# Kernel tuning notes

Hardware: AMD Instinct MI355X
Metric: run time of the kernel (lower is better)

The kernel has to match this reference:

```python
import jax, jax.numpy as jnp
import numpy as np
from jax import lax

M, N, Q = 256, 65536, 64
LAMBDA_STAR = 0.1
LAMBDA_O = 0.1
T_ITERS = 16
PM_ITERS = 100


def setup_inputs() -> dict:
    key = jax.random.key(0)
    kx, kd = jax.random.split(key)
    X = jax.random.normal(kx, (M, N), dtype=jnp.float32)
    D = jax.random.normal(kd, (M, Q), dtype=jnp.float32)
    return {"X": X, "D": D}


def _power_method(D):
    # Largest eigenvalue of D^T D via 100-step power iteration (fixed random init).
    x0 = jax.random.normal(jax.random.key(1), (1, Q), dtype=D.dtype)

    def step(x, _):
        x = (x @ D.T) @ D          # [1,q] -> [1,m] -> [1,q]
        nm = jnp.linalg.norm(x)
        return x / nm, nm

    _, nms = lax.scan(step, x0, None, length=PM_ITERS)
    return nms[-1]


def reference(X, D):
    m, n = X.shape
    q = D.shape[1]
    alpha = _power_method(D)
    eta = 1.0 / alpha

    Iq = jnp.eye(q, dtype=D.dtype)
    Im = jnp.eye(m, dtype=D.dtype)
    top = jnp.concatenate([D.T @ D + LAMBDA_STAR * Iq, D.T], axis=1)   # [q, q+m]
    bot = jnp.concatenate([D, (1.0 + LAMBDA_STAR) * Im], axis=1)       # [m, q+m]
    H = jnp.eye(m + q, dtype=D.dtype) - eta * jnp.concatenate([top, bot], axis=0)
    W = eta * jnp.concatenate([D.T, Im], axis=0)                        # [(m+q), m]
    t = LAMBDA_O * eta * jnp.concatenate([jnp.zeros(q, D.dtype), jnp.ones(m, D.dtype)])

    b0 = W @ X                                                           # [(m+q), n]
    Z0 = jnp.zeros((m + q, n), dtype=X.dtype)

    def ista_step(carry, _):
        Z, b = carry
        Znew = jnp.maximum(0.0, b - t[:, None])    # thresholding (ger(t, ones) == t broadcast)
        b = b + H @ (Znew - Z)
        return (Znew, b), None

    (Z, _), _ = lax.scan(ista_step, (Z0, b0), None, length=T_ITERS)
    return Z
```

## Files before the change

### kernel.cpp

```cpp
#include <hip/hip_runtime.h>


typedef __bf16 bf16x8 __attribute__((ext_vector_type(8)));
typedef __bf16 bf16x2 __attribute__((ext_vector_type(2)));
typedef float f32x4 __attribute__((ext_vector_type(4)));
typedef float f32x2 __attribute__((ext_vector_type(2)));

#define MFMA16(a, b, c) __builtin_amdgcn_mfma_f32_16x16x32_bf16((a), (b), (c), 0, 0, 0)

#define NTOT 65536
#define NCOL 32

__device__ __forceinline__ unsigned pk2(float a, float b) {
#if __has_builtin(__builtin_amdgcn_cvt_pk_bf16_f32)
  return __builtin_bit_cast(unsigned, __builtin_amdgcn_cvt_pk_bf16_f32(a, b));
#else
  unsigned short ua = __builtin_bit_cast(unsigned short, (__bf16)a);
  unsigned short ub = __builtin_bit_cast(unsigned short, (__bf16)b);
  return (unsigned)ua | ((unsigned)ub << 16);
#endif
}
__device__ __forceinline__ unsigned pk2v(f32x2 v) { return pk2(v[0], v[1]); }
__device__ __forceinline__ f32x2 f2(float s) { f32x2 v = {s, s}; return v; }
__device__ __forceinline__ f32x2 pfma(f32x2 a, f32x2 b, f32x2 c) {
  return __builtin_elementwise_fma(a, b, c);
}
__device__ __forceinline__ f32x2 pmax0(f32x2 a) {
  return __builtin_elementwise_max(a, f2(0.f));
}

#define GOF(row) ((row) * 68 + (((row) >> 3) << 2))
__global__ void rnmf_prep(const float* __restrict__ D, void* __restrict__ ws) {
  float* wsf = (float*)ws;
  __bf16* Dbf = (__bf16*)((char*)ws + 256);
  __bf16* DTbf = (__bf16*)((char*)ws + 256 + 32768);

  const int tid = threadIdx.x;

  if (blockIdx.x != 0) {
    const int bs = blockIdx.x - 1;
#pragma unroll
    for (int e = 0; e < 8; ++e) {
      int i4 = bs * 2048 + e * 256 + tid;
      float4 dv = *(const float4*)(D + i4 * 4);
      uint2 u; u.x = pk2(dv.x, dv.y); u.y = pk2(dv.z, dv.w);
      *(uint2*)(Dbf + i4 * 4) = u;
    }
    const int a = tid & 63;
#pragma unroll
    for (int e = 0; e < 4; ++e) {
      int kc = bs * 16 + e * 4 + (tid >> 6);
      int k0 = kc * 8;
      float g0 = D[(k0 + 0) * 64 + a], g1 = D[(k0 + 1) * 64 + a];
      float g2 = D[(k0 + 2) * 64 + a], g3 = D[(k0 + 3) * 64 + a];
      float g4 = D[(k0 + 4) * 64 + a], g5 = D[(k0 + 5) * 64 + a];
      float g6 = D[(k0 + 6) * 64 + a], g7 = D[(k0 + 7) * 64 + a];
      uint4 o;
      o.x = pk2(g0, g1); o.y = pk2(g2, g3); o.z = pk2(g4, g5); o.w = pk2(g6, g7);
      *(uint4*)(DTbf + a * 256 + k0) = o;
    }
    return;
  }

  __shared__ __bf16 DTl[64 * 264];
  __shared__ __bf16 gA[64 * 72];
  __shared__ __bf16 gB[64 * 72];
  __shared__ float gf[64 * 68 + 32];
  __shared__ __align__(16) float xv[64];

  const int w = tid >> 6, lane = tid & 63, c = lane & 15, q4 = lane >> 4;

#pragma unroll
  for (int e = 0; e < 64; ++e) {
    int flat = e * 256 + tid;
    int k = flat >> 6, a = flat & 63;
    DTl[a * 264 + k] = (__bf16)D[k * 64 + a];
  }
  __syncthreads();
#pragma unroll
  for (int ct = 0; ct < 4; ++ct) {
    f32x4 acc = {0.f, 0.f, 0.f, 0.f};
#pragma unroll
    for (int kb = 0; kb < 8; ++kb) {
      bf16x8 a = *(const bf16x8*)&DTl[(16 * w + c) * 264 + 32 * kb + 8 * q4];
      bf16x8 b = *(const bf16x8*)&DTl[(16 * ct + c) * 264 + 32 * kb + 8 * q4];
      acc = MFMA16(a, b, acc);
    }
#pragma unroll
    for (int r = 0; r < 4; ++r)
      gA[(16 * w + 4 * q4 + r) * 72 + 16 * ct + c] = (__bf16)acc[r];
  }
  __syncthreads();
#pragma unroll
  for (int ct = 0; ct < 4; ++ct) {
    f32x4 acc = {0.f, 0.f, 0.f, 0.f};
#pragma unroll
    for (int kb = 0; kb < 2; ++kb) {
      bf16x8 a = *(const bf16x8*)&gA[(16 * w + c) * 72 + 32 * kb + 8 * q4];
      bf16x8 b = *(const bf16x8*)&gA[(16 * ct + c) * 72 + 32 * kb + 8 * q4];
      acc = MFMA16(a, b, acc);
    }
#pragma unroll
    for (int r = 0; r < 4; ++r)
      gB[(16 * w + 4 * q4 + r) * 72 + 16 * ct + c] = (__bf16)acc[r];
  }
  __syncthreads();
#pragma unroll
  for (int ct = 0; ct < 4; ++ct) {
    f32x4 acc = {0.f, 0.f, 0.f, 0.f};
#pragma unroll
    for (int kb = 0; kb < 2; ++kb) {
      bf16x8 a = *(const bf16x8*)&gB[(16 * w + c) * 72 + 32 * kb + 8 * q4];
      bf16x8 b = *(const bf16x8*)&gB[(16 * ct + c) * 72 + 32 * kb + 8 * q4];
      acc = MFMA16(a, b, acc);
    }
#pragma unroll
    for (int r = 0; r < 4; ++r)
      gA[(16 * w + 4 * q4 + r) * 72 + 16 * ct + c] = (__bf16)acc[r];
  }
  __syncthreads();
#pragma unroll
  for (int ct = 0; ct < 4; ++ct) {
    f32x4 acc = {0.f, 0.f, 0.f, 0.f};
#pragma unroll
    for (int kb = 0; kb < 2; ++kb) {
      bf16x8 a = *(const bf16x8*)&gA[(16 * w + c) * 72 + 32 * kb + 8 * q4];
      bf16x8 b = *(const bf16x8*)&gA[(16 * ct + c) * 72 + 32 * kb + 8 * q4];
      acc = MFMA16(a, b, acc);
    }
#pragma unroll
    for (int r = 0; r < 4; ++r)
      gf[GOF(16 * w + 4 * q4 + r) + 16 * ct + c] = acc[r];
  }
  __syncthreads();

  if (w == 0) {
    float td = gf[GOF(lane) + lane];
#pragma unroll
    for (int off = 32; off; off >>= 1) td += __shfl_xor(td, off, 64);
    const float tr = td;
    const float itr = 1.f / tr;
    xv[lane] = 1.f;
    float nm = 1.f;
    const int rowoff = GOF(lane);
    for (int itp = 0; itp < 28; ++itp) {
      float a0 = 0.f, a1 = 0.f, a2 = 0.f, a3 = 0.f;
#pragma unroll
      for (int k = 0; k < 64; k += 16) {
        float4 ga = *(const float4*)&gf[rowoff + k];
        float4 xa = *(const float4*)&xv[k];
        float4 gb = *(const float4*)&gf[rowoff + k + 4];
        float4 xb = *(const float4*)&xv[k + 4];
        float4 gc = *(const float4*)&gf[rowoff + k + 8];
        float4 xc = *(const float4*)&xv[k + 8];
        float4 gd = *(const float4*)&gf[rowoff + k + 12];
        float4 xd = *(const float4*)&xv[k + 12];
        a0 = fmaf(ga.x, xa.x, a0); a0 = fmaf(ga.y, xa.y, a0);
        a0 = fmaf(ga.z, xa.z, a0); a0 = fmaf(ga.w, xa.w, a0);
        a1 = fmaf(gb.x, xb.x, a1); a1 = fmaf(gb.y, xb.y, a1);
        a1 = fmaf(gb.z, xb.z, a1); a1 = fmaf(gb.w, xb.w, a1);
        a2 = fmaf(gc.x, xc.x, a2); a2 = fmaf(gc.y, xc.y, a2);
        a2 = fmaf(gc.z, xc.z, a2); a2 = fmaf(gc.w, xc.w, a2);
        a3 = fmaf(gd.x, xd.x, a3); a3 = fmaf(gd.y, xd.y, a3);
        a3 = fmaf(gd.z, xd.z, a3); a3 = fmaf(gd.w, xd.w, a3);
      }
      float acc = (a0 + a1) + (a2 + a3);
      float y = acc * itr;
      float n2 = y * y;
#pragma unroll
      for (int off = 32; off; off >>= 1) n2 += __shfl_xor(n2, off, 64);
      nm = sqrtf(n2);
      xv[lane] = y / nm;
    }
    if (lane == 0) wsf[0] = 1.f / powf(nm * tr, 0.125f);
  }
}

__global__ __launch_bounds__(256, 2) void rnmf_main(const float* __restrict__ X,
                                                    float* __restrict__ Z,
                                                    const void* __restrict__ ws) {
  const float* wsf = (const float*)ws;
  const __bf16* Dbf = (const __bf16*)((const char*)ws + 256);
  const __bf16* DTbf = (const __bf16*)((const char*)ws + 256 + 32768);

  __shared__ __align__(16) char arena[33280];
  float* xs = (float*)arena;

  const int tid = threadIdx.x;
  const int w = tid >> 6;
  const int lane = tid & 63;
  const int c = lane & 15;
  const int q4 = lane >> 4;
  const int q4h = q4 >> 1, q4l = q4 & 1;
  const int wr = w >> 1, wc = w & 1;
  const int j0 = blockIdx.x * NCOL;

#pragma unroll
  for (int e = 0; e < 8; ++e) {
    int idx = e * 256 + tid;
    int row = idx >> 3, c4 = (idx & 7) * 4;
    float4 g = *(const float4*)(X + row * NTOT + j0 + c4);
    xs[(c4 + 0) * 260 + row] = g.x;
    xs[(c4 + 1) * 260 + row] = g.y;
    xs[(c4 + 2) * 260 + row] = g.z;
    xs[(c4 + 3) * 260 + row] = g.w;
  }

  const float eta = wsf[0];
  const f32x2 etav = f2(eta);
  const f32x2 metav = f2(-eta);
  const f32x2 cqv = f2(1.f - 0.1f * eta);
  const f32x2 cmv = f2(1.f - 1.1f * eta);
  const float tm = 0.1f * eta;

  bf16x8 d1[8][2];
#pragma unroll
  for (int rt = 0; rt < 8; ++rt)
#pragma unroll
    for (int kb = 0; kb < 2; ++kb)
      d1[rt][kb] = *(const bf16x8*)(Dbf + (128 * wr + 16 * rt + c) * 64 + 32 * kb + 8 * q4);
  bf16x8 d2[2][8];
#pragma unroll
  for (int rt2 = 0; rt2 < 2; ++rt2)
#pragma unroll
    for (int kb = 0; kb < 8; ++kb)
      d2[rt2][kb] = *(const bf16x8*)(DTbf + (32 * wr + 16 * rt2 + c) * 256 + 32 * kb + 8 * q4);

  __syncthreads();

  bf16x8 xb[8];
#pragma unroll
  for (int kb = 0; kb < 8; ++kb) {
    const float* p = &xs[(16 * wc + c) * 260 + 32 * kb + 8 * q4];
    float4 lo = *(const float4*)p;
    float4 hi = *(const float4*)(p + 4);
    uint4 packed = {pk2(lo.x, lo.y), pk2(lo.z, lo.w), pk2(hi.x, hi.y), pk2(hi.z, hi.w)};
    xb[kb] = __builtin_bit_cast(bf16x8, packed);
  }

  f32x2 bqt2[2][2];
#pragma unroll
  for (int rt2 = 0; rt2 < 2; ++rt2) {
    f32x4 acc = {0.f, 0.f, 0.f, 0.f};
#pragma unroll
    for (int kb = 0; kb < 8; ++kb) acc = MFMA16(d2[rt2][kb], xb[kb], acc);
    f32x2 a0 = {acc[0], acc[1]}, a1 = {acc[2], acc[3]};
    bqt2[rt2][0] = etav * a0;
    bqt2[rt2][1] = etav * a1;
  }

  f32x2 bmt2[8][2];
#pragma unroll
  for (int rt = 0; rt < 8; ++rt) {
    const float* p = &xs[(16 * wc + c) * 260 + 128 * wr + 16 * rt + 4 * q4];
    float4 v = *(const float4*)p;
    f32x2 x0 = {v.x, v.y}, x1 = {v.z, v.w};
    bmt2[rt][0] = pfma(etav, x0, f2(-tm));
    bmt2[rt][1] = pfma(etav, x1, f2(-tm));
  }

  __syncthreads();

  f32x2 zq2[2][2], zm2[8][2];
#pragma unroll
  for (int rt2 = 0; rt2 < 2; ++rt2)
#pragma unroll
    for (int p = 0; p < 2; ++p) zq2[rt2][p] = pmax0(bqt2[rt2][p]);
#pragma unroll
  for (int rt = 0; rt < 8; ++rt)
#pragma unroll
    for (int p = 0; p < 2; ++p) zm2[rt][p] = pmax0(bmt2[rt][p]);

  char* smem = arena;
  const int rb = lane * 16;
  const int zqrd = wc * 2048 + rb;
  const int vrd = 4096 + wc * 8192 + rb;
  const int wzq = wc * 2048 + wr * 1024 + q4h * 256 + c * 16 + 8 * q4l;
  const int wvb = 4096 + wc * 8192 + wr * 4096 + q4h * 256 + c * 16 + 8 * q4l;

#pragma unroll
  for (int rt2 = 0; rt2 < 2; ++rt2) {
    uint2 u; u.x = pk2v(zq2[rt2][0]); u.y = pk2v(zq2[rt2][1]);
    *(uint2*)(smem + wzq + rt2 * 512) = u;
  }

  for (int it = 0; it < 15; ++it) {
    __syncthreads();
    bf16x8 bz0 = *(const bf16x8*)(smem + zqrd);
    bf16x8 bz1 = *(const bf16x8*)(smem + zqrd + 1024);
#pragma unroll
    for (int rt = 0; rt < 8; ++rt) {
      f32x4 acc = {0.f, 0.f, 0.f, 0.f};
      acc = MFMA16(d1[rt][0], bz0, acc);
      acc = MFMA16(d1[rt][1], bz1, acc);
      f32x2 u0 = {acc[0], acc[1]}, u1 = {acc[2], acc[3]};
      f32x2 z0 = zm2[rt][0], z1v = zm2[rt][1];
      f32x2 v0 = u0 + z0, v1 = u1 + z1v;
      f32x2 t0 = pfma(cmv, z0, bmt2[rt][0]);
      f32x2 t1 = pfma(cmv, z1v, bmt2[rt][1]);
      zm2[rt][0] = pmax0(pfma(metav, u0, t0));
      zm2[rt][1] = pmax0(pfma(metav, u1, t1));
      uint2 uu; uu.x = pk2v(v0); uu.y = pk2v(v1);
      *(uint2*)(smem + wvb + rt * 512) = uu;
    }
    __syncthreads();
    f32x4 aA0 = {0.f, 0.f, 0.f, 0.f}, aA1 = {0.f, 0.f, 0.f, 0.f};
    f32x4 aB0 = {0.f, 0.f, 0.f, 0.f}, aB1 = {0.f, 0.f, 0.f, 0.f};
#pragma unroll
    for (int kb = 0; kb < 4; ++kb) {
      bf16x8 bv = *(const bf16x8*)(smem + vrd + kb * 1024);
      aA0 = MFMA16(d2[0][kb], bv, aA0);
      aA1 = MFMA16(d2[1][kb], bv, aA1);
    }
#pragma unroll
    for (int kb = 4; kb < 8; ++kb) {
      bf16x8 bv = *(const bf16x8*)(smem + vrd + kb * 1024);
      aB0 = MFMA16(d2[0][kb], bv, aB0);
      aB1 = MFMA16(d2[1][kb], bv, aB1);
    }
    f32x4 s0 = aA0 + aB0;
    f32x4 s1 = aA1 + aB1;
    {
      f32x2 w0 = {s0[0], s0[1]}, w1 = {s0[2], s0[3]};
      f32x2 t0 = pfma(cqv, zq2[0][0], bqt2[0][0]);
      f32x2 t1 = pfma(cqv, zq2[0][1], bqt2[0][1]);
      zq2[0][0] = pmax0(pfma(metav, w0, t0));
      zq2[0][1] = pmax0(pfma(metav, w1, t1));
      uint2 u; u.x = pk2v(zq2[0][0]); u.y = pk2v(zq2[0][1]);
      *(uint2*)(smem + wzq) = u;
    }
    {
      f32x2 w0 = {s1[0], s1[1]}, w1 = {s1[2], s1[3]};
      f32x2 t0 = pfma(cqv, zq2[1][0], bqt2[1][0]);
      f32x2 t1 = pfma(cqv, zq2[1][1], bqt2[1][1]);
      zq2[1][0] = pmax0(pfma(metav, w0, t0));
      zq2[1][1] = pmax0(pfma(metav, w1, t1));
      uint2 u; u.x = pk2v(zq2[1][0]); u.y = pk2v(zq2[1][1]);
      *(uint2*)(smem + wzq + 512) = u;
    }
  }

#pragma unroll
  for (int rt2 = 0; rt2 < 2; ++rt2)
#pragma unroll
    for (int p = 0; p < 2; ++p)
#pragma unroll
      for (int e = 0; e < 2; ++e)
        Z[(32 * wr + 16 * rt2 + 4 * q4 + 2 * p + e) * NTOT + j0 + 16 * wc + c] = zq2[rt2][p][e];
#pragma unroll
  for (int rt = 0; rt < 8; ++rt)
#pragma unroll
    for (int p = 0; p < 2; ++p)
#pragma unroll
      for (int e = 0; e < 2; ++e)
        Z[(64 + 128 * wr + 16 * rt + 4 * q4 + 2 * p + e) * NTOT + j0 + 16 * wc + c] = zm2[rt][p][e];
}

extern "C" void kernel_launch(void* const* d_in, const int* in_sizes, int n_in,
                              void* d_out, int out_size, void* d_ws, size_t ws_size,
                              hipStream_t stream) {
  const float* X = (const float*)d_in[0];
  const float* D = (const float*)d_in[1];
  float* Z = (float*)d_out;
  rnmf_prep<<<dim3(3), dim3(256), 0, stream>>>(D, d_ws);
  rnmf_main<<<dim3(NTOT / NCOL), dim3(256), 0, stream>>>(X, Z, d_ws);
}
```

Measured before the change: 224.4 us.

## Halve columns per block and repartition waves over rows only

Each block now handles 16 columns instead of 32, and the four waves split the row dimension (64 rows of D, 16 rows of D^T each) instead of a 2x2 row/column grid. Per-thread register state for D fragments and Z tiles is halved and shared memory drops to about 16 KB, which allows three blocks per CU and twice as many blocks. The cost is that each block reloads the same D fragments for half as much work, and global stores are narrower (16 consecutive floats per row).

```diff
diff --git a/kernel.cpp b/kernel.cpp
--- a/kernel.cpp
+++ b/kernel.cpp
@@ -2,14 +2,13 @@
 
 
 typedef __bf16 bf16x8 __attribute__((ext_vector_type(8)));
-typedef __bf16 bf16x2 __attribute__((ext_vector_type(2)));
 typedef float f32x4 __attribute__((ext_vector_type(4)));
 typedef float f32x2 __attribute__((ext_vector_type(2)));
 
 #define MFMA16(a, b, c) __builtin_amdgcn_mfma_f32_16x16x32_bf16((a), (b), (c), 0, 0, 0)
 
 #define NTOT 65536
-#define NCOL 32
+#define NCOL 16
 
 __device__ __forceinline__ unsigned pk2(float a, float b) {
 #if __has_builtin(__builtin_amdgcn_cvt_pk_bf16_f32)
@@ -176,15 +175,16 @@
   }
 }
 
-__global__ __launch_bounds__(256, 2) void rnmf_main(const float* __restrict__ X,
+__global__ __launch_bounds__(256, 3) void rnmf_main(const float* __restrict__ X,
                                                     float* __restrict__ Z,
                                                     const void* __restrict__ ws) {
   const float* wsf = (const float*)ws;
   const __bf16* Dbf = (const __bf16*)((const char*)ws + 256);
   const __bf16* DTbf = (const __bf16*)((const char*)ws + 256 + 32768);
 
-  __shared__ __align__(16) char arena[33280];
+  __shared__ __align__(16) char arena[16640];
   float* xs = (float*)arena;
+  char* smem = arena;
 
   const int tid = threadIdx.x;
   const int w = tid >> 6;
@@ -192,13 +192,12 @@
   const int c = lane & 15;
   const int q4 = lane >> 4;
   const int q4h = q4 >> 1, q4l = q4 & 1;
-  const int wr = w >> 1, wc = w & 1;
   const int j0 = blockIdx.x * NCOL;
 
 #pragma unroll
-  for (int e = 0; e < 8; ++e) {
+  for (int e = 0; e < 4; ++e) {
     int idx = e * 256 + tid;
-    int row = idx >> 3, c4 = (idx & 7) * 4;
+    int row = idx >> 2, c4 = (idx & 3) * 4;
     float4 g = *(const float4*)(X + row * NTOT + j0 + c4);
     xs[(c4 + 0) * 260 + row] = g.x;
     xs[(c4 + 1) * 260 + row] = g.y;
@@ -213,46 +212,46 @@
   const f32x2 cmv = f2(1.f - 1.1f * eta);
   const float tm = 0.1f * eta;
 
-  bf16x8 d1[8][2];
-#pragma unroll
-  for (int rt = 0; rt < 8; ++rt)
+  bf16x8 d1[4][2];
+#pragma unroll
+  for (int rt = 0; rt < 4; ++rt)
 #pragma unroll
     for (int kb = 0; kb < 2; ++kb)
-      d1[rt][kb] = *(const bf16x8*)(Dbf + (128 * wr + 16 * rt + c) * 64 + 32 * kb + 8 * q4);
-  bf16x8 d2[2][8];
-#pragma unroll
-  for (int rt2 = 0; rt2 < 2; ++rt2)
-#pragma unroll
-    for (int kb = 0; kb < 8; ++kb)
-      d2[rt2][kb] = *(const bf16x8*)(DTbf + (32 * wr + 16 * rt2 + c) * 256 + 32 * kb + 8 * q4);
+      d1[rt][kb] = *(const bf16x8*)(Dbf + (64 * w + 16 * rt + c) * 64 + 32 * kb + 8 * q4);
+  bf16x8 d2[8];
+#pragma unroll
+  for (int kb = 0; kb < 8; ++kb)
+    d2[kb] = *(const bf16x8*)(DTbf + (16 * w + c) * 256 + 32 * kb + 8 * q4);
 
   __syncthreads();
 
   bf16x8 xb[8];
 #pragma unroll
   for (int kb = 0; kb < 8; ++kb) {
-    const float* p = &xs[(16 * wc + c) * 260 + 32 * kb + 8 * q4];
+    const float* p = &xs[c * 260 + 32 * kb + 8 * q4];
     float4 lo = *(const float4*)p;
     float4 hi = *(const float4*)(p + 4);
     uint4 packed = {pk2(lo.x, lo.y), pk2(lo.z, lo.w), pk2(hi.x, hi.y), pk2(hi.z, hi.w)};
     xb[kb] = __builtin_bit_cast(bf16x8, packed);
   }
 
-  f32x2 bqt2[2][2];
-#pragma unroll
-  for (int rt2 = 0; rt2 < 2; ++rt2) {
-    f32x4 acc = {0.f, 0.f, 0.f, 0.f};
-#pragma unroll
-    for (int kb = 0; kb < 8; ++kb) acc = MFMA16(d2[rt2][kb], xb[kb], acc);
+  f32x2 bqt2[2];
+  {
+    f32x4 aA = {0.f, 0.f, 0.f, 0.f}, aB = {0.f, 0.f, 0.f, 0.f};
+#pragma unroll
+    for (int kb = 0; kb < 4; ++kb) aA = MFMA16(d2[kb], xb[kb], aA);
+#pragma unroll
+    for (int kb = 4; kb < 8; ++kb) aB = MFMA16(d2[kb], xb[kb], aB);
+    f32x4 acc = aA + aB;
     f32x2 a0 = {acc[0], acc[1]}, a1 = {acc[2], acc[3]};
-    bqt2[rt2][0] = etav * a0;
-    bqt2[rt2][1] = etav * a1;
-  }
-
-  f32x2 bmt2[8][2];
-#pragma unroll
-  for (int rt = 0; rt < 8; ++rt) {
-    const float* p = &xs[(16 * wc + c) * 260 + 128 * wr + 16 * rt + 4 * q4];
+    bqt2[0] = etav * a0;
+    bqt2[1] = etav * a1;
+  }
+
+  f32x2 bmt2[4][2];
+#pragma unroll
+  for (int rt = 0; rt < 4; ++rt) {
+    const float* p = &xs[c * 260 + 64 * w + 16 * rt + 4 * q4];
     float4 v = *(const float4*)p;
     f32x2 x0 = {v.x, v.y}, x1 = {v.z, v.w};
     bmt2[rt][0] = pfma(etav, x0, f2(-tm));
@@ -261,35 +260,30 @@
 
   __syncthreads();
 
-  f32x2 zq2[2][2], zm2[8][2];
-#pragma unroll
-  for (int rt2 = 0; rt2 < 2; ++rt2)
-#pragma unroll
-    for (int p = 0; p < 2; ++p) zq2[rt2][p] = pmax0(bqt2[rt2][p]);
-#pragma unroll
-  for (int rt = 0; rt < 8; ++rt)
+  f32x2 zq2[2], zm2[4][2];
+#pragma unroll
+  for (int p = 0; p < 2; ++p) zq2[p] = pmax0(bqt2[p]);
+#pragma unroll
+  for (int rt = 0; rt < 4; ++rt)
 #pragma unroll
     for (int p = 0; p < 2; ++p) zm2[rt][p] = pmax0(bmt2[rt][p]);
 
-  char* smem = arena;
   const int rb = lane * 16;
-  const int zqrd = wc * 2048 + rb;
-  const int vrd = 4096 + wc * 8192 + rb;
-  const int wzq = wc * 2048 + wr * 1024 + q4h * 256 + c * 16 + 8 * q4l;
-  const int wvb = 4096 + wc * 8192 + wr * 4096 + q4h * 256 + c * 16 + 8 * q4l;
-
-#pragma unroll
-  for (int rt2 = 0; rt2 < 2; ++rt2) {
-    uint2 u; u.x = pk2v(zq2[rt2][0]); u.y = pk2v(zq2[rt2][1]);
-    *(uint2*)(smem + wzq + rt2 * 512) = u;
+  const int vrd = 2048 + rb;
+  const int wzq = w * 512 + q4h * 256 + c * 16 + 8 * q4l;
+  const int wvb = 2048 + w * 2048 + q4h * 256 + c * 16 + 8 * q4l;
+
+  {
+    uint2 u; u.x = pk2v(zq2[0]); u.y = pk2v(zq2[1]);
+    *(uint2*)(smem + wzq) = u;
   }
 
   for (int it = 0; it < 15; ++it) {
     __syncthreads();
-    bf16x8 bz0 = *(const bf16x8*)(smem + zqrd);
-    bf16x8 bz1 = *(const bf16x8*)(smem + zqrd + 1024);
-#pragma unroll
-    for (int rt = 0; rt < 8; ++rt) {
+    bf16x8 bz0 = *(const bf16x8*)(smem + rb);
+    bf16x8 bz1 = *(const bf16x8*)(smem + rb + 1024);
+#pragma unroll
+    for (int rt = 0; rt < 4; ++rt) {
       f32x4 acc = {0.f, 0.f, 0.f, 0.f};
       acc = MFMA16(d1[rt][0], bz0, acc);
       acc = MFMA16(d1[rt][1], bz1, acc);
@@ -304,56 +298,39 @@
       *(uint2*)(smem + wvb + rt * 512) = uu;
     }
     __syncthreads();
-    f32x4 aA0 = {0.f, 0.f, 0.f, 0.f}, aA1 = {0.f, 0.f, 0.f, 0.f};
-    f32x4 aB0 = {0.f, 0.f, 0.f, 0.f}, aB1 = {0.f, 0.f, 0.f, 0.f};
+    f32x4 aA = {0.f, 0.f, 0.f, 0.f}, aB = {0.f, 0.f, 0.f, 0.f};
 #pragma unroll
     for (int kb = 0; kb < 4; ++kb) {
       bf16x8 bv = *(const bf16x8*)(smem + vrd + kb * 1024);
-      aA0 = MFMA16(d2[0][kb], bv, aA0);
-      aA1 = MFMA16(d2[1][kb], bv, aA1);
+      aA = MFMA16(d2[kb], bv, aA);
     }
 #pragma unroll
     for (int kb = 4; kb < 8; ++kb) {
       bf16x8 bv = *(const bf16x8*)(smem + vrd + kb * 1024);
-      aB0 = MFMA16(d2[0][kb], bv, aB0);
-      aB1 = MFMA16(d2[1][kb], bv, aB1);
-    }
-    f32x4 s0 = aA0 + aB0;
-    f32x4 s1 = aA1 + aB1;
-    {
-      f32x2 w0 = {s0[0], s0[1]}, w1 = {s0[2], s0[3]};
-      f32x2 t0 = pfma(cqv, zq2[0][0], bqt2[0][0]);
-      f32x2 t1 = pfma(cqv, zq2[0][1], bqt2[0][1]);
-      zq2[0][0] = pmax0(pfma(metav, w0, t0));
-      zq2[0][1] = pmax0(pfma(metav, w1, t1));
-      uint2 u; u.x = pk2v(zq2[0][0]); u.y = pk2v(zq2[0][1]);
-      *(uint2*)(smem + wzq) = u;
-    }
-    {
-      f32x2 w0 = {s1[0], s1[1]}, w1 = {s1[2], s1[3]};
-      f32x2 t0 = pfma(cqv, zq2[1][0], bqt2[1][0]);
-      f32x2 t1 = pfma(cqv, zq2[1][1], bqt2[1][1]);
-      zq2[1][0] = pmax0(pfma(metav, w0, t0));
-      zq2[1][1] = pmax0(pfma(metav, w1, t1));
-      uint2 u; u.x = pk2v(zq2[1][0]); u.y = pk2v(zq2[1][1]);
-      *(uint2*)(smem + wzq + 512) = u;
-    }
-  }
-
-#pragma unroll
-  for (int rt2 = 0; rt2 < 2; ++rt2)
+      aB = MFMA16(d2[kb], bv, aB);
+    }
+    f32x4 s = aA + aB;
+    f32x2 s0 = {s[0], s[1]}, s1 = {s[2], s[3]};
+    f32x2 t0 = pfma(cqv, zq2[0], bqt2[0]);
+    f32x2 t1 = pfma(cqv, zq2[1], bqt2[1]);
+    zq2[0] = pmax0(pfma(metav, s0, t0));
+    zq2[1] = pmax0(pfma(metav, s1, t1));
+    uint2 u; u.x = pk2v(zq2[0]); u.y = pk2v(zq2[1]);
+    *(uint2*)(smem + wzq) = u;
+  }
+
+#pragma unroll
+  for (int p = 0; p < 2; ++p)
+#pragma unroll
+    for (int e = 0; e < 2; ++e)
+      Z[(16 * w + 4 * q4 + 2 * p + e) * NTOT + j0 + c] = zq2[p][e];
+#pragma unroll
+  for (int rt = 0; rt < 4; ++rt)
 #pragma unroll
     for (int p = 0; p < 2; ++p)
 #pragma unroll
       for (int e = 0; e < 2; ++e)
-        Z[(32 * wr + 16 * rt2 + 4 * q4 + 2 * p + e) * NTOT + j0 + 16 * wc + c] = zq2[rt2][p][e];
-#pragma unroll
-  for (int rt = 0; rt < 8; ++rt)
-#pragma unroll
-    for (int p = 0; p < 2; ++p)
-#pragma unroll
-      for (int e = 0; e < 2; ++e)
-        Z[(64 + 128 * wr + 16 * rt + 4 * q4 + 2 * p + e) * NTOT + j0 + 16 * wc + c] = zm2[rt][p][e];
+        Z[(64 + 64 * w + 16 * rt + 4 * q4 + 2 * p + e) * NTOT + j0 + c] = zm2[rt][p][e];
 }
 
 extern "C" void kernel_launch(void* const* d_in, const int* in_sizes, int n_in,
```

After: 216.2 us. 3.7% less time.
